# Optimization experiments

Measured on AMD Instinct MI355X. Metric: run time of the kernel, lower is better.

Reference implementation:

```python
import jax, jax.numpy as jnp
import numpy as np

K = 3  # Chebyshev order (number of coefficients)


def setup_inputs() -> dict:
    key = jax.random.key(0)
    k1, k2, k3, k4 = jax.random.split(key, 4)
    B, nNode, c_in, T = 16, 512, 32, 64
    c_out = 64
    x = jax.random.normal(k1, (B, nNode, c_in, T), dtype=jnp.float32)
    # scaled Laplacian-like batched adjacency; scale keeps the Chebyshev
    # recursion numerically tame (spectral norm ~ O(1))
    adj = jax.random.normal(k2, (B, nNode, nNode), dtype=jnp.float32) * (1.0 / np.sqrt(nNode))
    # 1x1 conv params: weight [c_out, K*c_in], bias [c_out]
    W = jax.random.normal(k3, (c_out, K * c_in), dtype=jnp.float32) * 0.1
    b = jax.random.normal(k4, (c_out,), dtype=jnp.float32) * 0.1
    return {"x": x, "adj": adj, "W": W, "b": b}


def reference(x, adj, W, b):
    # x: [B, nNode, c_in, T] -> permute(0,2,1,3) -> [B, c_in, nNode, T]
    x = jnp.transpose(x, (0, 2, 1, 3))
    B, c_in, nNode, T = x.shape
    # Chebyshev recursion: L0 = I, L1 = adj, L_k = 2*adj@L_{k-1} - L_{k-2}
    L0 = jnp.broadcast_to(jnp.eye(nNode, dtype=x.dtype), (B, nNode, nNode))
    L1 = adj
    Ls = [L0, L1]
    for _ in range(2, K):
        L2 = 2.0 * jnp.matmul(adj, L1) - L0
        L0, L1 = L1, L2
        Ls.append(L2)
    Lap = jnp.stack(Ls, axis=1)              # [B, K, nNode, nNode]
    Lap = jnp.swapaxes(Lap, -1, -2)          # transpose(-1, -2)
    # einsum 'bcnl,bknq->bckql' then view [B, c_in*K, nNode, T]
    y = jnp.einsum('bcnl,bknq->bckql', x, Lap)  # [B, c_in, K, nNode, T]
    y = y.reshape(B, c_in * K, nNode, T)
    # 1x1 Conv2d: channel mixing + bias
    out = jnp.einsum('oc,bcnl->bonl', W, y) + b[None, :, None, None]
    return out
```

## Files before the change

### kernel.cpp

```cpp
#include <hip/hip_runtime.h>

typedef unsigned short u16;
typedef __bf16 v8bf __attribute__((ext_vector_type(8)));
typedef float f32x4 __attribute__((ext_vector_type(4)));
typedef u16 us8 __attribute__((ext_vector_type(8)));
typedef u16 us4 __attribute__((ext_vector_type(4)));

static __device__ __forceinline__ u16 f2bf(float f) {
  union { __bf16 h; u16 u; } cv;
  cv.h = (__bf16)f;
  return cv.u;
}

static __device__ __forceinline__ void gl_lds16(const u16* g, u16* l) {
  __builtin_amdgcn_global_load_lds(
      (const __attribute__((address_space(1))) unsigned int*)g,
      (__attribute__((address_space(3))) unsigned int*)l, 16, 0, 0);
}

__global__ __launch_bounds__(256)
void cvt_adjT_foldw_k(const float* __restrict__ adj, u16* __restrict__ adj_bf,
                      u16* __restrict__ adjT_bf, const float* __restrict__ W,
                      u16* __restrict__ Mb) {
  const int c0 = blockIdx.x * 64;
  const int r0 = blockIdx.y * 64;
  const int b = blockIdx.z;
  __shared__ u16 Ls[64][68];
  const int tid = threadIdx.x;
#pragma unroll
  for (int i = 0; i < 4; ++i) {
    const int idx = tid + 256 * i;
    const int r = idx >> 4;
    const int c4 = (idx & 15) * 4;
    const float4 v = *(const float4*)(adj + ((size_t)(b * 512 + r0 + r) * 512 + c0 + c4));
    us4 o;
    o[0] = f2bf(v.x); o[1] = f2bf(v.y); o[2] = f2bf(v.z); o[3] = f2bf(v.w);
    *(us4*)&Ls[r][c4] = o;
    *(us4*)(adj_bf + ((size_t)(b * 512 + r0 + r) * 512 + c0 + c4)) = o;
  }
  __syncthreads();
#pragma unroll
  for (int i = 0; i < 2; ++i) {
    const int idx = tid + 256 * i;
    const int c = idx >> 3;
    const int r8 = (idx & 7) * 8;
    us8 o;
#pragma unroll
    for (int j = 0; j < 8; ++j) o[j] = Ls[r8 + j][c];
    *(us8*)(adjT_bf + ((size_t)(b * 512 + c0 + c) * 512 + r0 + r8)) = o;
  }
  if (blockIdx.x == 0 && blockIdx.y == 0 && blockIdx.z == 0) {
    for (int i = tid; i < 64 * 96; i += 256) {
      const int cc = i % 96;
      const int r = cc % 3;
      const float w = W[i];
      const float m = (r == 0) ? (w - W[i + 2]) : w;
      Mb[i] = f2bf(m);
    }
  }
}

__global__ __launch_bounds__(256)
void cvtT_x_k(const float* __restrict__ x, u16* __restrict__ xT) {
  const int j0 = blockIdx.x * 64;
  const int q0 = blockIdx.y * 64;
  const int b = blockIdx.z;
  __shared__ u16 Ls[64][68];
  const int tid = threadIdx.x;
#pragma unroll
  for (int i = 0; i < 4; ++i) {
    const int idx = tid + 256 * i;
    const int r = idx >> 4;
    const int j4 = (idx & 15) * 4;
    const float4 v = *(const float4*)(x + ((size_t)(b * 512 + q0 + r) * 2048 + j0 + j4));
    us4 o;
    o[0] = f2bf(v.x); o[1] = f2bf(v.y); o[2] = f2bf(v.z); o[3] = f2bf(v.w);
    *(us4*)&Ls[r][j4] = o;
  }
  __syncthreads();
#pragma unroll
  for (int i = 0; i < 2; ++i) {
    const int idx = tid + 256 * i;
    const int jp = idx >> 3;
    const int q8 = (idx & 7) * 8;
    us8 o;
#pragma unroll
    for (int j = 0; j < 8; ++j) o[j] = Ls[q8 + j][jp];
    *(us8*)(xT + ((size_t)(b * 2048 + j0 + jp) * 512 + q0 + q8)) = o;
  }
}

__global__ __launch_bounds__(256)
void gemm_sq(const u16* __restrict__ A, const u16* __restrict__ BT,
             u16* __restrict__ C) {
  const int b = blockIdx.z;
  const int row0 = blockIdx.y * 128;
  const int col0 = blockIdx.x * 128;
  const u16* Ab = A + (size_t)b * 512 * 512;
  const u16* BTb = BT + (size_t)b * 512 * 512;

  __shared__ u16 smem[16384];
  u16* As = smem;
  u16* Bs = smem + 8192;

  const int tid = threadIdx.x;
  const int lane = tid & 63;
  const int w = tid >> 6;
  const int wm = (w >> 1) * 64;
  const int wn = (w & 1) * 64;
  const int l16 = lane & 15;
  const int kg = lane >> 4;

  f32x4 acc[4][4];
#pragma unroll
  for (int m = 0; m < 4; ++m)
#pragma unroll
    for (int n = 0; n < 4; ++n) acc[m][n] = (f32x4){0.f, 0.f, 0.f, 0.f};

  for (int k0 = 0; k0 < 512; k0 += 64) {
    __syncthreads();
#pragma unroll
    for (int i = 0; i < 4; ++i) {
      const int eb = w * 2048 + i * 512;
      const int e = eb + lane * 8;
      const int r = e >> 6;
      const int kk = e & 63;
      gl_lds16(Ab + (size_t)(row0 + r) * 512 + k0 + kk, As + eb);
      gl_lds16(BTb + (size_t)(col0 + r) * 512 + k0 + kk, Bs + eb);
    }
    __syncthreads();
#pragma unroll
    for (int ks = 0; ks < 2; ++ks) {
      v8bf af[4], bfr[4];
#pragma unroll
      for (int m = 0; m < 4; ++m)
        af[m] = *(const v8bf*)(As + (wm + m * 16 + l16) * 64 + ks * 32 + kg * 8);
#pragma unroll
      for (int n = 0; n < 4; ++n)
        bfr[n] = *(const v8bf*)(Bs + (wn + n * 16 + l16) * 64 + ks * 32 + kg * 8);
#pragma unroll
      for (int m = 0; m < 4; ++m)
#pragma unroll
        for (int n = 0; n < 4; ++n)
          acc[m][n] = __builtin_amdgcn_mfma_f32_16x16x32_bf16(af[m], bfr[n], acc[m][n], 0, 0, 0);
    }
  }
  u16* Cb = C + (size_t)b * 512 * 512;
#pragma unroll
  for (int m = 0; m < 4; ++m)
#pragma unroll
    for (int n = 0; n < 4; ++n)
#pragma unroll
      for (int v = 0; v < 4; ++v) {
        const int rr = row0 + wm + m * 16 + kg * 4 + v;
        const int cc = col0 + wn + n * 16 + l16;
        Cb[(size_t)rr * 512 + cc] = f2bf(2.0f * acc[m][n][v]);
      }
}

__global__ __launch_bounds__(512, 4)
void prop_k(const u16* __restrict__ A1, const u16* __restrict__ A2,
            const u16* __restrict__ BT, u16* __restrict__ X1,
            u16* __restrict__ Y2) {
  const int b = blockIdx.z;
  const int row0 = blockIdx.y * 128;
  const int col0 = blockIdx.x * 128;
  const u16* A1b = A1 + (size_t)b * 512 * 512;
  const u16* A2b = A2 + (size_t)b * 512 * 512;
  const u16* BTb = BT + (size_t)b * 2048 * 512;

  __shared__ u16 smem[24576];
  u16* As1 = smem;
  u16* As2 = smem + 8192;
  u16* Bs  = smem + 16384;

  const int tid = threadIdx.x;
  const int lane = tid & 63;
  const int w = tid >> 6;
  const int wq = w & 3;
  const int wm = (wq >> 1) * 64;
  const int wn = (wq & 1) * 64;
  const int l16 = lane & 15;
  const int kg = lane >> 4;

  f32x4 acc[4][4];
#pragma unroll
  for (int m = 0; m < 4; ++m)
#pragma unroll
    for (int n = 0; n < 4; ++n) acc[m][n] = (f32x4){0.f, 0.f, 0.f, 0.f};

  for (int k0 = 0; k0 < 512; k0 += 64) {
    __syncthreads();
#pragma unroll
    for (int i = 0; i < 2; ++i) {
      const int eb = w * 1024 + i * 512;
      const int e = eb + lane * 8;
      const int r = e >> 6;
      const int kk = e & 63;
      gl_lds16(A1b + (size_t)(row0 + r) * 512 + k0 + kk, As1 + eb);
      gl_lds16(A2b + (size_t)(row0 + r) * 512 + k0 + kk, As2 + eb);
      gl_lds16(BTb + (size_t)(col0 + r) * 512 + k0 + kk, Bs + eb);
    }
    __syncthreads();
    const u16* Asrc = (w < 4) ? As1 : As2;
#pragma unroll
    for (int ks = 0; ks < 2; ++ks) {
      v8bf af[4], bfr[4];
#pragma unroll
      for (int m = 0; m < 4; ++m)
        af[m] = *(const v8bf*)(Asrc + (wm + m * 16 + l16) * 64 + ks * 32 + kg * 8);
#pragma unroll
      for (int n = 0; n < 4; ++n)
        bfr[n] = *(const v8bf*)(Bs + (wn + n * 16 + l16) * 64 + ks * 32 + kg * 8);
#pragma unroll
      for (int m = 0; m < 4; ++m)
#pragma unroll
        for (int n = 0; n < 4; ++n)
          acc[m][n] = __builtin_amdgcn_mfma_f32_16x16x32_bf16(af[m], bfr[n], acc[m][n], 0, 0, 0);
    }
  }

  u16* Db = ((w < 4) ? X1 : Y2) + (size_t)b * 512 * 2048;
#pragma unroll
  for (int m = 0; m < 4; ++m)
#pragma unroll
    for (int n = 0; n < 4; ++n)
#pragma unroll
      for (int v = 0; v < 4; ++v) {
        const int rr = row0 + wm + m * 16 + kg * 4 + v;
        const int cc = col0 + wn + n * 16 + l16;
        Db[(size_t)rr * 2048 + cc] = f2bf(acc[m][n][v]);
      }
}

__global__ __launch_bounds__(256)
void mix_mfma(const float* __restrict__ x0, const u16* __restrict__ x1,
              const u16* __restrict__ y2, const u16* __restrict__ Mb,
              const float* __restrict__ bias, float* __restrict__ out) {
  const int q = blockIdx.x;
  const int b = blockIdx.y;
  __shared__ u16 Vt[64][104];
  __shared__ u16 Ms[64][104];
  const int tid = threadIdx.x;
  const int lane = tid & 63;
  const int w = tid >> 6;
  const int l16 = lane & 15;
  const int kg = lane >> 4;

#pragma unroll
  for (int i = 0; i < 3; ++i) {
    const int idx = tid + 256 * i;
    const int o = idx / 12;
    const int c8 = (idx % 12) * 8;
    *(uint4*)&Ms[o][c8] = *(const uint4*)(Mb + o * 96 + c8);
  }
  const size_t base = ((size_t)b * 512 + q) * 2048;
#pragma unroll
  for (int i = 0; i < 2; ++i) {
    const int idx = tid + 256 * i;
    const int c = idx >> 4;
    const int l0 = (idx & 15) * 4;
    const float4 v = *(const float4*)(x0 + base + c * 64 + l0);
    Vt[l0 + 0][3 * c] = f2bf(v.x);
    Vt[l0 + 1][3 * c] = f2bf(v.y);
    Vt[l0 + 2][3 * c] = f2bf(v.z);
    Vt[l0 + 3][3 * c] = f2bf(v.w);
  }
  {
    const int c = tid >> 3;
    const int l0 = (tid & 7) * 8;
    const us8 v1 = *(const us8*)(x1 + base + c * 64 + l0);
    const us8 v2 = *(const us8*)(y2 + base + c * 64 + l0);
#pragma unroll
    for (int j = 0; j < 8; ++j) {
      Vt[l0 + j][3 * c + 1] = v1[j];
      Vt[l0 + j][3 * c + 2] = v2[j];
    }
  }
  __syncthreads();

  f32x4 acc[4];
#pragma unroll
  for (int n = 0; n < 4; ++n) acc[n] = (f32x4){0.f, 0.f, 0.f, 0.f};
#pragma unroll
  for (int ks = 0; ks < 3; ++ks) {
    const v8bf a = *(const v8bf*)&Ms[w * 16 + l16][ks * 32 + kg * 8];
#pragma unroll
    for (int n = 0; n < 4; ++n) {
      const v8bf bv = *(const v8bf*)&Vt[n * 16 + l16][ks * 32 + kg * 8];
      acc[n] = __builtin_amdgcn_mfma_f32_16x16x32_bf16(a, bv, acc[n], 0, 0, 0);
    }
  }
#pragma unroll
  for (int n = 0; n < 4; ++n)
#pragma unroll
    for (int v = 0; v < 4; ++v) {
      const int o = w * 16 + kg * 4 + v;
      out[(((size_t)b * 64 + o) * 512 + q) * 64 + n * 16 + l16] = acc[n][v] + bias[o];
    }
}

extern "C" void kernel_launch(void* const* d_in, const int* in_sizes, int n_in,
                              void* d_out, int out_size, void* d_ws, size_t ws_size,
                              hipStream_t stream) {
  const float* x   = (const float*)d_in[0];
  const float* adj = (const float*)d_in[1];
  const float* W   = (const float*)d_in[2];
  const float* bia = (const float*)d_in[3];
  float* out = (float*)d_out;

  u16* adj_bf  = (u16*)d_ws;
  u16* adjT_bf = adj_bf  + (size_t)16 * 512 * 512;
  u16* adj2_bf = adjT_bf + (size_t)16 * 512 * 512;
  u16* xT      = adj2_bf + (size_t)16 * 512 * 512;
  u16* X1      = xT      + (size_t)16 * 2048 * 512;
  u16* Y2      = X1      + (size_t)16 * 512 * 2048;
  u16* Mb      = Y2      + (size_t)16 * 512 * 2048;

  hipLaunchKernelGGL(cvt_adjT_foldw_k, dim3(8, 8, 16), dim3(256), 0, stream,
                     adj, adj_bf, adjT_bf, W, Mb);
  hipLaunchKernelGGL(cvtT_x_k, dim3(32, 8, 16), dim3(256), 0, stream, x, xT);
  hipLaunchKernelGGL(gemm_sq, dim3(4, 4, 16), dim3(256), 0, stream,
                     adj_bf, adjT_bf, adj2_bf);
  hipLaunchKernelGGL(prop_k, dim3(16, 4, 16), dim3(512), 0, stream,
                     adj_bf, adj2_bf, xT, X1, Y2);
  hipLaunchKernelGGL(mix_mfma, dim3(512, 16), dim3(256), 0, stream,
                     x, X1, Y2, Mb, bia, out);
}
```

Before: 152.8 us.

## Merge prep kernels and double-buffer prop GEMM with remapped block order

Merges the adj and x conversion/transpose kernels into one launch, saving a kernel launch and tail gap. In prop_k, uses a k-major LDS layout with K-step 32 and double-buffered global_load_lds prefetch, so loads overlap the MFMAs and one barrier is dropped per step. It also raises wave priority around the MFMA block and remaps block ids so consecutive blocks land on different XCDs while sharing batch data. The shorter K-step doubles the iteration count, and the new LDS layout may add bank conflicts.

```diff
diff --git a/kernel.cpp b/kernel.cpp
--- a/kernel.cpp
+++ b/kernel.cpp
@@ -19,37 +19,66 @@
 }
 
 __global__ __launch_bounds__(256)
-void cvt_adjT_foldw_k(const float* __restrict__ adj, u16* __restrict__ adj_bf,
-                      u16* __restrict__ adjT_bf, const float* __restrict__ W,
-                      u16* __restrict__ Mb) {
-  const int c0 = blockIdx.x * 64;
-  const int r0 = blockIdx.y * 64;
-  const int b = blockIdx.z;
+void prep_k(const float* __restrict__ adj, u16* __restrict__ adj_bf,
+            u16* __restrict__ adjT_bf, const float* __restrict__ x,
+            u16* __restrict__ xT, const float* __restrict__ W,
+            u16* __restrict__ Mb) {
+  const int bid = blockIdx.x;
+  const int tid = threadIdx.x;
   __shared__ u16 Ls[64][68];
-  const int tid = threadIdx.x;
-#pragma unroll
-  for (int i = 0; i < 4; ++i) {
-    const int idx = tid + 256 * i;
-    const int r = idx >> 4;
-    const int c4 = (idx & 15) * 4;
-    const float4 v = *(const float4*)(adj + ((size_t)(b * 512 + r0 + r) * 512 + c0 + c4));
-    us4 o;
-    o[0] = f2bf(v.x); o[1] = f2bf(v.y); o[2] = f2bf(v.z); o[3] = f2bf(v.w);
-    *(us4*)&Ls[r][c4] = o;
-    *(us4*)(adj_bf + ((size_t)(b * 512 + r0 + r) * 512 + c0 + c4)) = o;
-  }
-  __syncthreads();
-#pragma unroll
-  for (int i = 0; i < 2; ++i) {
-    const int idx = tid + 256 * i;
-    const int c = idx >> 3;
-    const int r8 = (idx & 7) * 8;
-    us8 o;
-#pragma unroll
-    for (int j = 0; j < 8; ++j) o[j] = Ls[r8 + j][c];
-    *(us8*)(adjT_bf + ((size_t)(b * 512 + c0 + c) * 512 + r0 + r8)) = o;
-  }
-  if (blockIdx.x == 0 && blockIdx.y == 0 && blockIdx.z == 0) {
+  if (bid < 1024) {
+    const int b = bid >> 6;
+    const int r0 = ((bid >> 3) & 7) * 64;
+    const int c0 = (bid & 7) * 64;
+#pragma unroll
+    for (int i = 0; i < 4; ++i) {
+      const int idx = tid + 256 * i;
+      const int r = idx >> 4;
+      const int c4 = (idx & 15) * 4;
+      const float4 v = *(const float4*)(adj + ((size_t)(b * 512 + r0 + r) * 512 + c0 + c4));
+      us4 o;
+      o[0] = f2bf(v.x); o[1] = f2bf(v.y); o[2] = f2bf(v.z); o[3] = f2bf(v.w);
+      *(us4*)&Ls[r][c4] = o;
+      *(us4*)(adj_bf + ((size_t)(b * 512 + r0 + r) * 512 + c0 + c4)) = o;
+    }
+    __syncthreads();
+#pragma unroll
+    for (int i = 0; i < 2; ++i) {
+      const int idx = tid + 256 * i;
+      const int c = idx >> 3;
+      const int r8 = (idx & 7) * 8;
+      us8 o;
+#pragma unroll
+      for (int j = 0; j < 8; ++j) o[j] = Ls[r8 + j][c];
+      *(us8*)(adjT_bf + ((size_t)(b * 512 + c0 + c) * 512 + r0 + r8)) = o;
+    }
+  } else if (bid < 5120) {
+    const int t = bid - 1024;
+    const int b = t >> 8;
+    const int q0 = ((t >> 5) & 7) * 64;
+    const int j0 = (t & 31) * 64;
+#pragma unroll
+    for (int i = 0; i < 4; ++i) {
+      const int idx = tid + 256 * i;
+      const int r = idx >> 4;
+      const int j4 = (idx & 15) * 4;
+      const float4 v = *(const float4*)(x + ((size_t)(b * 512 + q0 + r) * 2048 + j0 + j4));
+      us4 o;
+      o[0] = f2bf(v.x); o[1] = f2bf(v.y); o[2] = f2bf(v.z); o[3] = f2bf(v.w);
+      *(us4*)&Ls[r][j4] = o;
+    }
+    __syncthreads();
+#pragma unroll
+    for (int i = 0; i < 2; ++i) {
+      const int idx = tid + 256 * i;
+      const int jp = idx >> 3;
+      const int q8 = (idx & 7) * 8;
+      us8 o;
+#pragma unroll
+      for (int j = 0; j < 8; ++j) o[j] = Ls[q8 + j][jp];
+      *(us8*)(xT + ((size_t)(b * 2048 + j0 + jp) * 512 + q0 + q8)) = o;
+    }
+  } else {
     for (int i = tid; i < 64 * 96; i += 256) {
       const int cc = i % 96;
       const int r = cc % 3;
@@ -57,36 +86,6 @@
       const float m = (r == 0) ? (w - W[i + 2]) : w;
       Mb[i] = f2bf(m);
     }
-  }
-}
-
-__global__ __launch_bounds__(256)
-void cvtT_x_k(const float* __restrict__ x, u16* __restrict__ xT) {
-  const int j0 = blockIdx.x * 64;
-  const int q0 = blockIdx.y * 64;
-  const int b = blockIdx.z;
-  __shared__ u16 Ls[64][68];
-  const int tid = threadIdx.x;
-#pragma unroll
-  for (int i = 0; i < 4; ++i) {
-    const int idx = tid + 256 * i;
-    const int r = idx >> 4;
-    const int j4 = (idx & 15) * 4;
-    const float4 v = *(const float4*)(x + ((size_t)(b * 512 + q0 + r) * 2048 + j0 + j4));
-    us4 o;
-    o[0] = f2bf(v.x); o[1] = f2bf(v.y); o[2] = f2bf(v.z); o[3] = f2bf(v.w);
-    *(us4*)&Ls[r][j4] = o;
-  }
-  __syncthreads();
-#pragma unroll
-  for (int i = 0; i < 2; ++i) {
-    const int idx = tid + 256 * i;
-    const int jp = idx >> 3;
-    const int q8 = (idx & 7) * 8;
-    us8 o;
-#pragma unroll
-    for (int j = 0; j < 8; ++j) o[j] = Ls[q8 + j][jp];
-    *(us8*)(xT + ((size_t)(b * 2048 + j0 + jp) * 512 + q0 + q8)) = o;
   }
 }
 
@@ -162,17 +161,17 @@
 void prop_k(const u16* __restrict__ A1, const u16* __restrict__ A2,
             const u16* __restrict__ BT, u16* __restrict__ X1,
             u16* __restrict__ Y2) {
-  const int b = blockIdx.z;
-  const int row0 = blockIdx.y * 128;
-  const int col0 = blockIdx.x * 128;
+  const int fid = blockIdx.x + 16 * (blockIdx.y + 4 * blockIdx.z);
+  const int wk = (fid & 7) * 128 + (fid >> 3);
+  const int b = wk >> 6;
+  const int row0 = ((wk >> 4) & 3) * 128;
+  const int col0 = (wk & 15) * 128;
+
   const u16* A1b = A1 + (size_t)b * 512 * 512;
   const u16* A2b = A2 + (size_t)b * 512 * 512;
   const u16* BTb = BT + (size_t)b * 2048 * 512;
 
-  __shared__ u16 smem[24576];
-  u16* As1 = smem;
-  u16* As2 = smem + 8192;
-  u16* Bs  = smem + 16384;
+  __shared__ u16 smem[2][3][4096];
 
   const int tid = threadIdx.x;
   const int lane = tid & 63;
@@ -183,41 +182,49 @@
   const int l16 = lane & 15;
   const int kg = lane >> 4;
 
+  const int sc = w * 64 + lane;
+  const int skg = sc >> 7;
+  const int srow = sc & 127;
+  const int sdst = sc * 8;
+  const size_t sA = (size_t)(row0 + srow) * 512 + skg * 8;
+  const size_t sB = (size_t)(col0 + srow) * 512 + skg * 8;
+
   f32x4 acc[4][4];
 #pragma unroll
   for (int m = 0; m < 4; ++m)
 #pragma unroll
     for (int n = 0; n < 4; ++n) acc[m][n] = (f32x4){0.f, 0.f, 0.f, 0.f};
 
-  for (int k0 = 0; k0 < 512; k0 += 64) {
-    __syncthreads();
-#pragma unroll
-    for (int i = 0; i < 2; ++i) {
-      const int eb = w * 1024 + i * 512;
-      const int e = eb + lane * 8;
-      const int r = e >> 6;
-      const int kk = e & 63;
-      gl_lds16(A1b + (size_t)(row0 + r) * 512 + k0 + kk, As1 + eb);
-      gl_lds16(A2b + (size_t)(row0 + r) * 512 + k0 + kk, As2 + eb);
-      gl_lds16(BTb + (size_t)(col0 + r) * 512 + k0 + kk, Bs + eb);
-    }
-    __syncthreads();
-    const u16* Asrc = (w < 4) ? As1 : As2;
-#pragma unroll
-    for (int ks = 0; ks < 2; ++ks) {
-      v8bf af[4], bfr[4];
-#pragma unroll
-      for (int m = 0; m < 4; ++m)
-        af[m] = *(const v8bf*)(Asrc + (wm + m * 16 + l16) * 64 + ks * 32 + kg * 8);
+  gl_lds16(A1b + sA, &smem[0][0][sdst]);
+  gl_lds16(A2b + sA, &smem[0][1][sdst]);
+  gl_lds16(BTb + sB, &smem[0][2][sdst]);
+  __syncthreads();
+
+  for (int t = 0; t < 16; ++t) {
+    const int cur = t & 1;
+    if (t < 15) {
+      const int k0 = (t + 1) * 32;
+      gl_lds16(A1b + sA + k0, &smem[cur ^ 1][0][sdst]);
+      gl_lds16(A2b + sA + k0, &smem[cur ^ 1][1][sdst]);
+      gl_lds16(BTb + sB + k0, &smem[cur ^ 1][2][sdst]);
+    }
+    const u16* As = (w < 4) ? smem[cur][0] : smem[cur][1];
+    const u16* Bs = smem[cur][2];
+    v8bf af[4], bfr[4];
+#pragma unroll
+    for (int m = 0; m < 4; ++m)
+      af[m] = *(const v8bf*)(As + (kg * 128 + wm + m * 16 + l16) * 8);
+#pragma unroll
+    for (int n = 0; n < 4; ++n)
+      bfr[n] = *(const v8bf*)(Bs + (kg * 128 + wn + n * 16 + l16) * 8);
+    __builtin_amdgcn_s_setprio(1);
+#pragma unroll
+    for (int m = 0; m < 4; ++m)
 #pragma unroll
       for (int n = 0; n < 4; ++n)
-        bfr[n] = *(const v8bf*)(Bs + (wn + n * 16 + l16) * 64 + ks * 32 + kg * 8);
-#pragma unroll
-      for (int m = 0; m < 4; ++m)
-#pragma unroll
-        for (int n = 0; n < 4; ++n)
-          acc[m][n] = __builtin_amdgcn_mfma_f32_16x16x32_bf16(af[m], bfr[n], acc[m][n], 0, 0, 0);
-    }
+        acc[m][n] = __builtin_amdgcn_mfma_f32_16x16x32_bf16(af[m], bfr[n], acc[m][n], 0, 0, 0);
+    __builtin_amdgcn_s_setprio(0);
+    __syncthreads();
   }
 
   u16* Db = ((w < 4) ? X1 : Y2) + (size_t)b * 512 * 2048;
@@ -317,9 +324,8 @@
   u16* Y2      = X1      + (size_t)16 * 512 * 2048;
   u16* Mb      = Y2      + (size_t)16 * 512 * 2048;
 
-  hipLaunchKernelGGL(cvt_adjT_foldw_k, dim3(8, 8, 16), dim3(256), 0, stream,
-                     adj, adj_bf, adjT_bf, W, Mb);
-  hipLaunchKernelGGL(cvtT_x_k, dim3(32, 8, 16), dim3(256), 0, stream, x, xT);
+  hipLaunchKernelGGL(prep_k, dim3(5121), dim3(256), 0, stream,
+                     adj, adj_bf, adjT_bf, x, xT, W, Mb);
   hipLaunchKernelGGL(gemm_sq, dim3(4, 4, 16), dim3(256), 0, stream,
                      adj_bf, adjT_bf, adj2_bf);
   hipLaunchKernelGGL(prop_k, dim3(16, 4, 16), dim3(512), 0, stream,
```

New measurement: 161.9 us. +5.9%, slower.
